# Optimization experiments

Measured on AMD Instinct MI355X. Metric: run time of the kernel, lower is better.

The kernel has to match this reference:

```python
import jax, jax.numpy as jnp
import numpy as np

D_MODEL = 1024
N_HEADS = 16
D_HEAD = D_MODEL // N_HEADS
D_FF = 4096
EPS = 1e-5


def _layernorm(x, g, b):
    mu = jnp.mean(x, axis=-1, keepdims=True)
    var = jnp.mean(jnp.square(x - mu), axis=-1, keepdims=True)
    return (x - mu) * jax.lax.rsqrt(var + EPS) * g + b


def setup_inputs() -> dict:
    key = jax.random.key(0)
    ks = jax.random.split(key, 16)
    B, S, D = 2, 2048, D_MODEL

    def xavier(k, shape):
        fan_in, fan_out = shape[0], shape[1]
        lim = float(np.sqrt(6.0 / (fan_in + fan_out)))
        return jax.random.uniform(k, shape, jnp.float32, -lim, lim)

    return {
        "x": jax.random.normal(ks[0], (B, S, D), jnp.float32),
        "ln1_g": jnp.ones((D,), jnp.float32),
        "ln1_b": jnp.zeros((D,), jnp.float32),
        "wq": xavier(ks[1], (D, D)), "bq": jnp.zeros((D,), jnp.float32),
        "wk": xavier(ks[2], (D, D)), "bk": jnp.zeros((D,), jnp.float32),
        "wv": xavier(ks[3], (D, D)), "bv": jnp.zeros((D,), jnp.float32),
        "wo": xavier(ks[4], (D, D)), "bo": jnp.zeros((D,), jnp.float32),
        "wf": xavier(ks[5], (D, N_HEADS)), "bf": jnp.zeros((N_HEADS,), jnp.float32),
        "ln2_g": jnp.ones((D,), jnp.float32),
        "ln2_b": jnp.zeros((D,), jnp.float32),
        "w1": xavier(ks[6], (D, D_FF)), "b1": jnp.zeros((D_FF,), jnp.float32),
        "w2": xavier(ks[7], (D_FF, D)), "b2": jnp.zeros((D,), jnp.float32),
    }


def reference(x, ln1_g, ln1_b, wq, bq, wk, bk, wv, bv, wo, bo, wf, bf,
              ln2_g, ln2_b, w1, b1, w2, b2):
    B, S, D = x.shape
    H, Dh = N_HEADS, D_HEAD

    # --- pre-norm forgetting attention ---
    h = _layernorm(x, ln1_g, ln1_b)
    q = (h @ wq + bq).reshape(B, S, H, Dh)
    k = (h @ wk + bk).reshape(B, S, H, Dh)
    v = (h @ wv + bv).reshape(B, S, H, Dh)

    # per-head scalar forget gate f_t in (0,1); cumulative log-decay c_t
    logf = jax.nn.log_sigmoid(h @ wf + bf)           # (B, S, H)
    c = jnp.cumsum(logf, axis=1)                     # (B, S, H)

    scale = 1.0 / jnp.sqrt(jnp.asarray(Dh, x.dtype))
    logits = jnp.einsum("bihd,bjhd->bhij", q, k) * scale
    # decay bias D_ij = c_i - c_j (sum of log forget gates in (j, i])
    decay = c.transpose(0, 2, 1)                     # (B, H, S)
    logits = logits + decay[:, :, :, None] - decay[:, :, None, :]

    causal = jnp.tril(jnp.ones((S, S), bool))
    logits = jnp.where(causal[None, None], logits, -jnp.inf)

    attn = jax.nn.softmax(logits, axis=-1)           # (B, H, S, S)
    ctx = jnp.einsum("bhij,bjhd->bihd", attn, v).reshape(B, S, D)
    attn_out = ctx @ wo + bo

    x = x + attn_out                                 # dropout = identity (eval)

    # --- pre-norm GELU MLP ---
    h2 = _layernorm(x, ln2_g, ln2_b)
    ff = jax.nn.gelu(h2 @ w1 + b1, approximate=False) @ w2 + b2
    return x + ff
```

## Files before the change

kernel.cpp:

```cpp
#include <hip/hip_runtime.h>
#include <hip/hip_bf16.h>
#include <math.h>

typedef unsigned short u16;
typedef unsigned int u32;
typedef __bf16 bf16x8 __attribute__((ext_vector_type(8)));
typedef float f32x4 __attribute__((ext_vector_type(4)));
typedef u32 u32x4 __attribute__((ext_vector_type(4)));

__device__ __forceinline__ u16 f2bf(float f) {
  __hip_bfloat16 h = __float2bfloat16(f);
  return *reinterpret_cast<u16*>(&h);
}
__device__ __forceinline__ float bf2f(u16 u) {
  return __uint_as_float(((u32)u) << 16);
}

#define GLL(gp, lp)                                                     \
  __builtin_amdgcn_global_load_lds(                                     \
      (const __attribute__((address_space(1))) void*)(gp),              \
      (__attribute__((address_space(3))) void*)(lp), 16, 0, 0)

__global__ __launch_bounds__(256) void transpose_cast(
    const float* __restrict__ in, u16* __restrict__ out, int R, int C) {
  __shared__ float tile[32][33];
  int c0 = blockIdx.x * 32, r0 = blockIdx.y * 32;
  int tx = threadIdx.x & 31, ty = threadIdx.x >> 5;
  for (int i = ty; i < 32; i += 8) {
    int r = r0 + i, c = c0 + tx;
    if (r < R && c < C) tile[i][tx] = in[(size_t)r * C + c];
  }
  __syncthreads();
  for (int i = ty; i < 32; i += 8) {
    int c = c0 + i, r = r0 + tx;
    if (c < C && r < R) out[(size_t)c * R + r] = f2bf(tile[tx][i]);
  }
}

__global__ __launch_bounds__(256) void pack3(
    const float* __restrict__ a, const float* __restrict__ b,
    const float* __restrict__ c, float* __restrict__ o, u32* __restrict__ ctr) {
  int t = blockIdx.x * 256 + threadIdx.x;
  if (t == 0) *ctr = 0u;
  if (t < 1024) o[t] = a[t];
  else if (t < 2048) o[t] = b[t - 1024];
  else if (t < 3072) o[t] = c[t - 2048];
}

__global__ __launch_bounds__(256) void ln_kernel(
    const float* __restrict__ x, const float* __restrict__ g,
    const float* __restrict__ bb, u16* __restrict__ out) {
  __shared__ float red[8];
  const int row = blockIdx.x;
  const float* xr = x + (size_t)row * 1024;
  f32x4 v = *(const f32x4*)(xr + threadIdx.x * 4);
  float s = v[0] + v[1] + v[2] + v[3];
  #pragma unroll
  for (int off = 32; off > 0; off >>= 1) s += __shfl_xor(s, off, 64);
  if ((threadIdx.x & 63) == 0) red[threadIdx.x >> 6] = s;
  __syncthreads();
  float mu = (red[0] + red[1] + red[2] + red[3]) * (1.0f / 1024.0f);
  f32x4 d;
  d[0] = v[0] - mu; d[1] = v[1] - mu; d[2] = v[2] - mu; d[3] = v[3] - mu;
  float sq = d[0]*d[0] + d[1]*d[1] + d[2]*d[2] + d[3]*d[3];
  #pragma unroll
  for (int off = 32; off > 0; off >>= 1) sq += __shfl_xor(sq, off, 64);
  if ((threadIdx.x & 63) == 0) red[4 + (threadIdx.x >> 6)] = sq;
  __syncthreads();
  float var = (red[4] + red[5] + red[6] + red[7]) * (1.0f / 1024.0f);
  float rstd = rsqrtf(var + 1e-5f);
  int cb = threadIdx.x * 4;
  #pragma unroll
  for (int e = 0; e < 4; ++e)
    out[(size_t)row * 1024 + cb + e] = f2bf(d[e] * rstd * g[cb + e] + bb[cb + e]);
}

__global__ __launch_bounds__(256) void gemm_bt(
    const u16* __restrict__ A, const u16* __restrict__ Bt,
    const float* __restrict__ bias, const float* __restrict__ res,
    void* __restrict__ outp, int M, int N, int K, int mode) {
  __shared__ u16 As[128 * 32];
  __shared__ u16 Bs[128 * 32];
  const int tid = threadIdx.x;
  const int m0 = blockIdx.y * 128, n0 = blockIdx.x * 128;
  const int wave = tid >> 6, lane = tid & 63;
  const int wm = (wave >> 1) * 64, wn = (wave & 1) * 64;
  const int lr = lane & 15, quad = lane >> 4;
  const int g0 = wave * 2;
  const int srow0 = g0 * 16 + (lane >> 2);
  const int scol = (lane & 3) * 8;
  const u16* Ag0 = A + (size_t)(m0 + srow0) * K + scol;
  const u16* Ag1 = A + (size_t)(m0 + srow0 + 16) * K + scol;
  const u16* Bg0 = Bt + (size_t)(n0 + srow0) * K + scol;
  const u16* Bg1 = Bt + (size_t)(n0 + srow0 + 16) * K + scol;
  u16* Al0 = As + g0 * 512;
  u16* Al1 = As + (g0 + 1) * 512;
  u16* Bl0 = Bs + g0 * 512;
  u16* Bl1 = Bs + (g0 + 1) * 512;

  f32x4 acc[4][4] = {};

  for (int k0 = 0; k0 < K; k0 += 32) {
    GLL(Ag0 + k0, Al0);
    GLL(Ag1 + k0, Al1);
    GLL(Bg0 + k0, Bl0);
    GLL(Bg1 + k0, Bl1);
    __syncthreads();
    bf16x8 af[4], bfr[4];
    #pragma unroll
    for (int t = 0; t < 4; ++t) {
      af[t]  = *(const bf16x8*)&As[(wm + t * 16 + lr) * 32 + quad * 8];
      bfr[t] = *(const bf16x8*)&Bs[(wn + t * 16 + lr) * 32 + quad * 8];
    }
    #pragma unroll
    for (int mt = 0; mt < 4; ++mt)
      #pragma unroll
      for (int nt = 0; nt < 4; ++nt)
        acc[mt][nt] = __builtin_amdgcn_mfma_f32_16x16x32_bf16(
            af[mt], bfr[nt], acc[mt][nt], 0, 0, 0);
    __syncthreads();
  }

  #pragma unroll
  for (int mt = 0; mt < 4; ++mt) {
    #pragma unroll
    for (int nt = 0; nt < 4; ++nt) {
      const int col = n0 + wn + nt * 16 + lr;
      const float bvv = bias[col];
      #pragma unroll
      for (int rr = 0; rr < 4; ++rr) {
        const int row = m0 + wm + mt * 16 + quad * 4 + rr;
        const size_t idx = (size_t)row * N + col;
        float v = acc[mt][nt][rr] + bvv;
        if (mode == 0) {
          ((float*)outp)[idx] = v;
        } else if (mode == 1) {
          ((float*)outp)[idx] = v + res[idx];
        } else if (mode == 2) {
          float gl = 0.5f * v * (1.0f + erff(v * 0.70710678118654752f));
          ((u16*)outp)[idx] = f2bf(gl);
        } else {
          ((u16*)outp)[idx] = f2bf(v);
        }
      }
    }
  }
}

__global__ __launch_bounds__(256) void gemm_n64(
    const u16* __restrict__ A, const u16* __restrict__ Bt,
    const float* __restrict__ bias, const float* __restrict__ res,
    void* __restrict__ outp, int M, int N, int K, int mode) {
  __shared__ u16 As[128 * 32];
  __shared__ u16 Bs[64 * 32];
  const int tid = threadIdx.x;
  const int m0 = blockIdx.y * 128, n0 = blockIdx.x * 64;
  const int wave = tid >> 6, lane = tid & 63;
  const int wm = (wave >> 1) * 64, wn = (wave & 1) * 32;
  const int lr = lane & 15, quad = lane >> 4;
  const int g0 = wave * 2;
  const int srow = lane >> 2;
  const int scol = (lane & 3) * 8;
  const u16* Ag0 = A + (size_t)(m0 + g0 * 16 + srow) * K + scol;
  const u16* Ag1 = A + (size_t)(m0 + g0 * 16 + 16 + srow) * K + scol;
  const u16* Bg  = Bt + (size_t)(n0 + wave * 16 + srow) * K + scol;
  u16* Al0 = As + g0 * 512;
  u16* Al1 = As + (g0 + 1) * 512;
  u16* Bl  = Bs + wave * 512;

  f32x4 acc[4][2] = {};

  for (int k0 = 0; k0 < K; k0 += 32) {
    GLL(Ag0 + k0, Al0);
    GLL(Ag1 + k0, Al1);
    GLL(Bg + k0, Bl);
    __syncthreads();
    bf16x8 af[4], bfr[2];
    #pragma unroll
    for (int t = 0; t < 4; ++t)
      af[t] = *(const bf16x8*)&As[(wm + t * 16 + lr) * 32 + quad * 8];
    #pragma unroll
    for (int t = 0; t < 2; ++t)
      bfr[t] = *(const bf16x8*)&Bs[(wn + t * 16 + lr) * 32 + quad * 8];
    #pragma unroll
    for (int mt = 0; mt < 4; ++mt)
      #pragma unroll
      for (int nt = 0; nt < 2; ++nt)
        acc[mt][nt] = __builtin_amdgcn_mfma_f32_16x16x32_bf16(
            af[mt], bfr[nt], acc[mt][nt], 0, 0, 0);
    __syncthreads();
  }

  #pragma unroll
  for (int mt = 0; mt < 4; ++mt) {
    #pragma unroll
    for (int nt = 0; nt < 2; ++nt) {
      const int col = n0 + wn + nt * 16 + lr;
      const float bvv = bias[col];
      #pragma unroll
      for (int rr = 0; rr < 4; ++rr) {
        const int row = m0 + wm + mt * 16 + quad * 4 + rr;
        const size_t idx = (size_t)row * N + col;
        float v = acc[mt][nt][rr] + bvv;
        if (mode == 0) {
          ((float*)outp)[idx] = v;
        } else if (mode == 1) {
          ((float*)outp)[idx] = v + res[idx];
        } else if (mode == 2) {
          float gl = 0.5f * v * (1.0f + erff(v * 0.70710678118654752f));
          ((u16*)outp)[idx] = f2bf(gl);
        } else {
          ((u16*)outp)[idx] = f2bf(v);
        }
      }
    }
  }
}

__global__ __launch_bounds__(64) void logf_kernel(
    const u16* __restrict__ h, const u16* __restrict__ wfT,
    const float* __restrict__ bfv, float* __restrict__ c) {
  const int row = blockIdx.x;
  const int lane = threadIdx.x;
  float acc[16];
  #pragma unroll
  for (int n = 0; n < 16; ++n) acc[n] = 0.f;
  for (int t = 0; t < 16; ++t) {
    int kidx = t * 64 + lane;
    float hv = bf2f(h[(size_t)row * 1024 + kidx]);
    #pragma unroll
    for (int n = 0; n < 16; ++n)
      acc[n] += hv * bf2f(wfT[n * 1024 + kidx]);
  }
  float z = 0.f;
  #pragma unroll
  for (int n = 0; n < 16; ++n) {
    float r = acc[n];
    #pragma unroll
    for (int off = 1; off < 64; off <<= 1) r += __shfl_xor(r, off, 64);
    if (lane == n) z = r;
  }
  if (lane < 16) {
    z += bfv[lane];
    float lf = (z >= 0.f) ? -log1pf(expf(-z)) : (z - log1pf(expf(z)));
    c[(size_t)row * 16 + lane] = lf;
  }
}

__global__ __launch_bounds__(64) void cumsum_kernel(float* __restrict__ c, int S) {
  const int b = blockIdx.x >> 4, h = blockIdx.x & 15;
  const int lane = threadIdx.x;
  float carry = 0.f;
  for (int s0 = 0; s0 < S; s0 += 64) {
    float v = c[(size_t)(b * S + s0 + lane) * 16 + h];
    #pragma unroll
    for (int off = 1; off < 64; off <<= 1) {
      float t = __shfl_up(v, off, 64);
      if (lane >= off) v += t;
    }
    v += carry;
    c[(size_t)(b * S + s0 + lane) * 16 + h] = v;
    carry = __shfl(v, 63, 64);
  }
}

__global__ __launch_bounds__(256) void vtrans(
    const u16* __restrict__ qkvb, u16* __restrict__ vtg) {
  __shared__ u16 t[32][33];
  const int bh = blockIdx.z, b = bh >> 4, h = bh & 15;
  const int s0 = blockIdx.x * 32, d0 = blockIdx.y * 32;
  const int tx = threadIdx.x & 31, ty = threadIdx.x >> 5;
  for (int i = ty; i < 32; i += 8)
    t[i][tx] = qkvb[(size_t)(b * 2048 + s0 + i) * 3072 + 2048 + h * 64 + d0 + tx];
  __syncthreads();
  for (int i = ty; i < 32; i += 8)
    vtg[(size_t)(bh * 64 + d0 + i) * 2048 + s0 + tx] = t[tx][i];
}

#define FS 72
#define NITEMS 1024
#define L2E 1.4426950408889634f

__global__ __launch_bounds__(256) void fattn(
    const u16* __restrict__ qkvb, const u16* __restrict__ vtg,
    const float* __restrict__ c, u16* __restrict__ ctx, u32* __restrict__ ctr) {
  __shared__ u16 Qs[64 * FS];
  __shared__ u16 Ks[64 * FS];
  __shared__ u16 Vt[64 * FS];
  __shared__ u16 Ps[64 * FS];
  __shared__ float cjs[64];
  __shared__ u32 sh_item;
  const int S = 2048;
  const int tid = threadIdx.x, wave = tid >> 6, lane = tid & 63;
  const int lr = lane & 15, quad = lane >> 4;
  const int w16 = wave * 16;
  const int sr = tid >> 2, scc = (tid & 3) * 16;

  for (;;) {
    if (tid == 0) sh_item = atomicAdd(ctr, 1u);
    __syncthreads();
    const u32 item = sh_item;
    if (item >= NITEMS) return;
    const int qt = 31 - (int)(item >> 5);
    const int bh = (int)(item & 31), b = bh >> 4, h = bh & 15;
    const int i0 = qt * 64;

    {
      const u16* src = qkvb + (size_t)(b * S + i0 + sr) * 3072 + h * 64 + scc;
      *(u32x4*)&Qs[sr * FS + scc] = *(const u32x4*)src;
      *(u32x4*)&Qs[sr * FS + scc + 8] = *(const u32x4*)(src + 8);
    }
    u32x4 kr0, kr1, vr0, vr1;
    float cjr = 0.f;
    {
      const u16* ks = qkvb + (size_t)(b * S + sr) * 3072 + 1024 + h * 64 + scc;
      kr0 = *(const u32x4*)ks;
      kr1 = *(const u32x4*)(ks + 8);
      const u16* vs = vtg + (size_t)(bh * 64 + sr) * 2048 + scc;
      vr0 = *(const u32x4*)vs;
      vr1 = *(const u32x4*)(vs + 8);
      if (tid < 64) cjr = c[(size_t)(b * S + tid) * 16 + h];
    }
    float ci[4], m_[4], l_[4], alpha[4];
    f32x4 o_[4];
    #pragma unroll
    for (int r = 0; r < 4; ++r) {
      ci[r] = c[(size_t)(b * S + i0 + w16 + quad * 4 + r) * 16 + h] * L2E;
      m_[r] = -INFINITY;
      l_[r] = 0.f;
    }
    #pragma unroll
    for (int dt = 0; dt < 4; ++dt) o_[dt] = (f32x4){0.f, 0.f, 0.f, 0.f};

    __syncthreads();
    const bf16x8 aq0 = *(const bf16x8*)&Qs[(w16 + lr) * FS + quad * 8];
    const bf16x8 aq1 = *(const bf16x8*)&Qs[(w16 + lr) * FS + 32 + quad * 8];

    const int ntiles = qt + 1;
    for (int jt = 0; jt < ntiles; ++jt) {
      const int j0 = jt * 64;
      *(u32x4*)&Ks[sr * FS + scc] = kr0;
      *(u32x4*)&Ks[sr * FS + scc + 8] = kr1;
      *(u32x4*)&Vt[sr * FS + scc] = vr0;
      *(u32x4*)&Vt[sr * FS + scc + 8] = vr1;
      if (tid < 64) cjs[tid] = cjr * L2E;
      if (jt + 1 < ntiles) {
        const int j1 = j0 + 64;
        const u16* ks = qkvb + (size_t)(b * S + j1 + sr) * 3072 + 1024 + h * 64 + scc;
        kr0 = *(const u32x4*)ks;
        kr1 = *(const u32x4*)(ks + 8);
        const u16* vs = vtg + (size_t)(bh * 64 + sr) * 2048 + j1 + scc;
        vr0 = *(const u32x4*)vs;
        vr1 = *(const u32x4*)(vs + 8);
        if (tid < 64) cjr = c[(size_t)(b * S + j1 + tid) * 16 + h];
      }
      __syncthreads();

      f32x4 sc[4];
      #pragma unroll
      for (int nt = 0; nt < 4; ++nt) {
        bf16x8 bk0 = *(const bf16x8*)&Ks[(nt * 16 + lr) * FS + quad * 8];
        bf16x8 bk1 = *(const bf16x8*)&Ks[(nt * 16 + lr) * FS + 32 + quad * 8];
        f32x4 z = {0.f, 0.f, 0.f, 0.f};
        z = __builtin_amdgcn_mfma_f32_16x16x32_bf16(aq0, bk0, z, 0, 0, 0);
        z = __builtin_amdgcn_mfma_f32_16x16x32_bf16(aq1, bk1, z, 0, 0, 0);
        sc[nt] = z;
      }
      const bool diag = (jt == qt);
      #pragma unroll
      for (int r = 0; r < 4; ++r) {
        const int i = i0 + w16 + quad * 4 + r;
        float lg[4], mrow = -INFINITY;
        #pragma unroll
        for (int nt = 0; nt < 4; ++nt) {
          const int j = j0 + nt * 16 + lr;
          float v = sc[nt][r] * (0.125f * L2E) + ci[r] - cjs[nt * 16 + lr];
          if (diag && (j > i)) v = -INFINITY;
          lg[nt] = v;
          mrow = fmaxf(mrow, v);
        }
        #pragma unroll
        for (int off = 1; off < 16; off <<= 1)
          mrow = fmaxf(mrow, __shfl_xor(mrow, off, 64));
        const float mn = fmaxf(m_[r], mrow);
        alpha[r] = __builtin_exp2f(m_[r] - mn);
        m_[r] = mn;
        float rs = 0.f;
        #pragma unroll
        for (int nt = 0; nt < 4; ++nt) {
          const float p = __builtin_exp2f(lg[nt] - mn);
          Ps[(w16 + quad * 4 + r) * FS + nt * 16 + lr] = f2bf(p);
          rs += p;
        }
        l_[r] = l_[r] * alpha[r] + rs;
      }
      asm volatile("s_waitcnt lgkmcnt(0)" ::: "memory");
      #pragma unroll
      for (int dt = 0; dt < 4; ++dt)
        #pragma unroll
        for (int r = 0; r < 4; ++r) o_[dt][r] *= alpha[r];
      bf16x8 ap0 = *(const bf16x8*)&Ps[(w16 + lr) * FS + quad * 8];
      bf16x8 ap1 = *(const bf16x8*)&Ps[(w16 + lr) * FS + 32 + quad * 8];
      #pragma unroll
      for (int dt = 0; dt < 4; ++dt) {
        bf16x8 bv0 = *(const bf16x8*)&Vt[(dt * 16 + lr) * FS + quad * 8];
        bf16x8 bv1 = *(const bf16x8*)&Vt[(dt * 16 + lr) * FS + 32 + quad * 8];
        o_[dt] = __builtin_amdgcn_mfma_f32_16x16x32_bf16(ap0, bv0, o_[dt], 0, 0, 0);
        o_[dt] = __builtin_amdgcn_mfma_f32_16x16x32_bf16(ap1, bv1, o_[dt], 0, 0, 0);
      }
      __syncthreads();
    }
    #pragma unroll
    for (int r = 0; r < 4; ++r) {
      float lt = l_[r];
      #pragma unroll
      for (int off = 1; off < 16; off <<= 1) lt += __shfl_xor(lt, off, 64);
      const float inv = 1.0f / lt;
      const size_t base = (size_t)(b * S + i0 + w16 + quad * 4 + r) * 1024 + h * 64;
      #pragma unroll
      for (int dt = 0; dt < 4; ++dt)
        ctx[base + dt * 16 + lr] = f2bf(o_[dt][r] * inv);
    }
  }
}

extern "C" void kernel_launch(void* const* d_in, const int* in_sizes, int n_in,
                              void* d_out, int out_size, void* d_ws, size_t ws_size,
                              hipStream_t stream) {
  const float* x    = (const float*)d_in[0];
  const float* ln1g = (const float*)d_in[1];
  const float* ln1b = (const float*)d_in[2];
  const float* wq   = (const float*)d_in[3];
  const float* bq   = (const float*)d_in[4];
  const float* wk   = (const float*)d_in[5];
  const float* bk   = (const float*)d_in[6];
  const float* wv   = (const float*)d_in[7];
  const float* bv   = (const float*)d_in[8];
  const float* wo   = (const float*)d_in[9];
  const float* bo   = (const float*)d_in[10];
  const float* wf   = (const float*)d_in[11];
  const float* bfv  = (const float*)d_in[12];
  const float* ln2g = (const float*)d_in[13];
  const float* ln2b = (const float*)d_in[14];
  const float* w1   = (const float*)d_in[15];
  const float* b1   = (const float*)d_in[16];
  const float* w2   = (const float*)d_in[17];
  const float* b2   = (const float*)d_in[18];
  float* out = (float*)d_out;

  char* ws = (char*)d_ws;
  const size_t MB = 1024 * 1024;
  u16*   wqkvT = (u16*)(ws + 0 * MB);
  u16*   woT   = (u16*)(ws + 6 * MB);
  u16*   w1T   = (u16*)(ws + 8 * MB);
  u16*   w2T   = (u16*)(ws + 16 * MB);
  u16*   wfT   = (u16*)(ws + 24 * MB);
  float* bqkv  = (float*)(ws + 24 * MB + 65536);
  u32*   fctr  = (u32*)(ws + 24 * MB + 131072);
  u16*   hbuf  = (u16*)(ws + 25 * MB);
  u16*   ctx   = (u16*)(ws + 33 * MB);
  u16*   qkvb  = (u16*)(ws + 41 * MB);
  u16*   vtg   = (u16*)(ws + 65 * MB);
  float* cb    = (float*)(ws + 73 * MB);
  u16*   act1  = (u16*)(ws + 74 * MB);

  dim3 blk(256);
  transpose_cast<<<dim3(32, 32), blk, 0, stream>>>(wq, wqkvT, 1024, 1024);
  transpose_cast<<<dim3(32, 32), blk, 0, stream>>>(wk, wqkvT + 1024 * 1024, 1024, 1024);
  transpose_cast<<<dim3(32, 32), blk, 0, stream>>>(wv, wqkvT + 2 * 1024 * 1024, 1024, 1024);
  transpose_cast<<<dim3(32, 32), blk, 0, stream>>>(wo, woT, 1024, 1024);
  transpose_cast<<<dim3(128, 32), blk, 0, stream>>>(w1, w1T, 1024, 4096);
  transpose_cast<<<dim3(32, 128), blk, 0, stream>>>(w2, w2T, 4096, 1024);
  transpose_cast<<<dim3(1, 32), blk, 0, stream>>>(wf, wfT, 1024, 16);
  pack3<<<12, blk, 0, stream>>>(bq, bk, bv, bqkv, fctr);
  ln_kernel<<<4096, blk, 0, stream>>>(x, ln1g, ln1b, hbuf);
  gemm_bt<<<dim3(24, 32), blk, 0, stream>>>(hbuf, wqkvT, bqkv, nullptr, qkvb,
                                            4096, 3072, 1024, 3);
  logf_kernel<<<4096, dim3(64), 0, stream>>>(hbuf, wfT, bfv, cb);
  cumsum_kernel<<<32, dim3(64), 0, stream>>>(cb, 2048);
  vtrans<<<dim3(64, 2, 32), blk, 0, stream>>>(qkvb, vtg);
  fattn<<<dim3(512), blk, 0, stream>>>(qkvb, vtg, cb, ctx, fctr);
  gemm_n64<<<dim3(16, 32), blk, 0, stream>>>(ctx, woT, bo, x, out,
                                             4096, 1024, 1024, 1);
  ln_kernel<<<4096, blk, 0, stream>>>(out, ln2g, ln2b, hbuf);
  gemm_bt<<<dim3(32, 32), blk, 0, stream>>>(hbuf, w1T, b1, nullptr, act1,
                                            4096, 4096, 1024, 2);
  gemm_n64<<<dim3(16, 32), blk, 0, stream>>>(act1, w2T, b2, out, out,
                                             4096, 1024, 4096, 1);
}
```

Measured before the change: 524.0 us.

## Skip decayed attention tiles, split-K the FFN down-projection, fuse residual into LN2

The attention kernel now walks key tiles from the diagonal backwards. It drops the query-side decay term and stops early once a bound built from the max Q/K norms and the cumulative decay says the remaining logits fall more than 40 below the running max. This removes work on tiles whose weights are negligible, at the cost of an approximation with a fixed threshold. A new qk_norms kernel computes per-tile norm maxima, and the persistent grid doubles to 1024 blocks. The second LayerNorm also writes x+b2 into the output, so the FFN down GEMM becomes a 4-way split-K with atomic float adds, trading more parallelism for atomic traffic and nondeterministic summation order.

```diff
diff --git a/kernel.cpp b/kernel.cpp
--- a/kernel.cpp
+++ b/kernel.cpp
@@ -48,8 +48,9 @@
 }
 
 __global__ __launch_bounds__(256) void ln_kernel(
-    const float* __restrict__ x, const float* __restrict__ g,
-    const float* __restrict__ bb, u16* __restrict__ out) {
+    const float* x, const float* __restrict__ g,
+    const float* __restrict__ bb, u16* __restrict__ out,
+    float* xadd, const float* addb) {
   __shared__ float red[8];
   const int row = blockIdx.x;
   const float* xr = x + (size_t)row * 1024;
@@ -73,6 +74,12 @@
   #pragma unroll
   for (int e = 0; e < 4; ++e)
     out[(size_t)row * 1024 + cb + e] = f2bf(d[e] * rstd * g[cb + e] + bb[cb + e]);
+  if (xadd) {
+    f32x4 w;
+    #pragma unroll
+    for (int e = 0; e < 4; ++e) w[e] = v[e] + addb[cb + e];
+    *(f32x4*)(xadd + (size_t)row * 1024 + cb) = w;
+  }
 }
 
 __global__ __launch_bounds__(256) void gemm_bt(
@@ -217,6 +224,65 @@
   }
 }
 
+__global__ __launch_bounds__(256) void gemm_n64_sk(
+    const u16* __restrict__ A, const u16* __restrict__ Bt,
+    float* __restrict__ outp, int M, int N, int Ktot, int Kslice) {
+  __shared__ u16 As[128 * 32];
+  __shared__ u16 Bs[64 * 32];
+  const int tid = threadIdx.x;
+  const int m0 = blockIdx.y * 128, n0 = blockIdx.x * 64;
+  const int kbeg = blockIdx.z * Kslice, kend = kbeg + Kslice;
+  const int wave = tid >> 6, lane = tid & 63;
+  const int wm = (wave >> 1) * 64, wn = (wave & 1) * 32;
+  const int lr = lane & 15, quad = lane >> 4;
+  const int g0 = wave * 2;
+  const int srow = lane >> 2;
+  const int scol = (lane & 3) * 8;
+  const u16* Ag0 = A + (size_t)(m0 + g0 * 16 + srow) * Ktot + scol;
+  const u16* Ag1 = A + (size_t)(m0 + g0 * 16 + 16 + srow) * Ktot + scol;
+  const u16* Bg  = Bt + (size_t)(n0 + wave * 16 + srow) * Ktot + scol;
+  u16* Al0 = As + g0 * 512;
+  u16* Al1 = As + (g0 + 1) * 512;
+  u16* Bl  = Bs + wave * 512;
+
+  f32x4 acc[4][2] = {};
+
+  for (int k0 = kbeg; k0 < kend; k0 += 32) {
+    GLL(Ag0 + k0, Al0);
+    GLL(Ag1 + k0, Al1);
+    GLL(Bg + k0, Bl);
+    __syncthreads();
+    bf16x8 af[4], bfr[2];
+    #pragma unroll
+    for (int t = 0; t < 4; ++t)
+      af[t] = *(const bf16x8*)&As[(wm + t * 16 + lr) * 32 + quad * 8];
+    #pragma unroll
+    for (int t = 0; t < 2; ++t)
+      bfr[t] = *(const bf16x8*)&Bs[(wn + t * 16 + lr) * 32 + quad * 8];
+    #pragma unroll
+    for (int mt = 0; mt < 4; ++mt)
+      #pragma unroll
+      for (int nt = 0; nt < 2; ++nt)
+        acc[mt][nt] = __builtin_amdgcn_mfma_f32_16x16x32_bf16(
+            af[mt], bfr[nt], acc[mt][nt], 0, 0, 0);
+    __syncthreads();
+  }
+
+  #pragma unroll
+  for (int mt = 0; mt < 4; ++mt) {
+    #pragma unroll
+    for (int nt = 0; nt < 2; ++nt) {
+      const int col = n0 + wn + nt * 16 + lr;
+      #pragma unroll
+      for (int rr = 0; rr < 4; ++rr) {
+        const int row = m0 + wm + mt * 16 + quad * 4 + rr;
+        __hip_atomic_fetch_add(&outp[(size_t)row * N + col], acc[mt][nt][rr],
+                               __ATOMIC_RELAXED, __HIP_MEMORY_SCOPE_AGENT);
+      }
+    }
+  }
+}
+
 __global__ __launch_bounds__(64) void logf_kernel(
     const u16* __restrict__ h, const u16* __restrict__ wfT,
     const float* __restrict__ bfv, float* __restrict__ c) {
@@ -277,18 +343,46 @@
     vtg[(size_t)(bh * 64 + d0 + i) * 2048 + s0 + tx] = t[tx][i];
 }
 
+__global__ __launch_bounds__(64) void qk_norms(
+    const u16* __restrict__ qkvb, float* __restrict__ qkmax) {
+  const int tile = blockIdx.x, bh = blockIdx.y, z = blockIdx.z;
+  const int b = bh >> 4, h = bh & 15;
+  const int tok = tile * 64 + (int)threadIdx.x;
+  const u16* p = qkvb + (size_t)(b * 2048 + tok) * 3072 + z * 1024 + h * 64;
+  float s = 0.f;
+  #pragma unroll
+  for (int i = 0; i < 4; ++i) {
+    u32x4 w = *(const u32x4*)(p + i * 16);
+    u32x4 w2 = *(const u32x4*)(p + i * 16 + 8);
+    #pragma unroll
+    for (int e = 0; e < 4; ++e) {
+      float lo = __uint_as_float(w[e] << 16);
+      float hi = __uint_as_float(w[e] & 0xffff0000u);
+      float lo2 = __uint_as_float(w2[e] << 16);
+      float hi2 = __uint_as_float(w2[e] & 0xffff0000u);
+      s += lo * lo + hi * hi + lo2 * lo2 + hi2 * hi2;
+    }
+  }
+  s = sqrtf(s);
+  #pragma unroll
+  for (int off = 1; off < 64; off <<= 1) s = fmaxf(s, __shfl_xor(s, off, 64));
+  if (threadIdx.x == 0) qkmax[z * 1024 + bh * 32 + tile] = s;
+}
+
 #define FS 72
 #define NITEMS 1024
 #define L2E 1.4426950408889634f
 
 __global__ __launch_bounds__(256) void fattn(
     const u16* __restrict__ qkvb, const u16* __restrict__ vtg,
-    const float* __restrict__ c, u16* __restrict__ ctx, u32* __restrict__ ctr) {
+    const float* __restrict__ c, const float* __restrict__ qkmax,
+    u16* __restrict__ ctx, u32* __restrict__ ctr) {
   __shared__ u16 Qs[64 * FS];
   __shared__ u16 Ks[64 * FS];
   __shared__ u16 Vt[64 * FS];
   __shared__ u16 Ps[64 * FS];
   __shared__ float cjs[64];
+  __shared__ float wmn[4];
   __shared__ u32 sh_item;
   const int S = 2048;
   const int tid = threadIdx.x, wave = tid >> 6, lane = tid & 63;
@@ -313,19 +407,25 @@
     u32x4 kr0, kr1, vr0, vr1;
     float cjr = 0.f;
     {
-      const u16* ks = qkvb + (size_t)(b * S + sr) * 3072 + 1024 + h * 64 + scc;
+      const u16* ks = qkvb + (size_t)(b * S + i0 + sr) * 3072 + 1024 + h * 64 + scc;
       kr0 = *(const u32x4*)ks;
       kr1 = *(const u32x4*)(ks + 8);
-      const u16* vs = vtg + (size_t)(bh * 64 + sr) * 2048 + scc;
+      const u16* vs = vtg + (size_t)(bh * 64 + sr) * 2048 + i0 + scc;
       vr0 = *(const u32x4*)vs;
       vr1 = *(const u32x4*)(vs + 8);
-      if (tid < 64) cjr = c[(size_t)(b * S + tid) * 16 + h];
-    }
-    float ci[4], m_[4], l_[4], alpha[4];
+      if (tid < 64) cjr = c[(size_t)(b * S + i0 + tid) * 16 + h];
+    }
+    float bscale;
+    {
+      float qm = qkmax[bh * 32 + qt];
+      float km = 0.f;
+      for (int t = 0; t <= qt; ++t) km = fmaxf(km, qkmax[1024 + bh * 32 + t]);
+      bscale = qm * km * (0.125f * L2E);
+    }
+    float m_[4], l_[4], alpha[4];
     f32x4 o_[4];
     #pragma unroll
     for (int r = 0; r < 4; ++r) {
-      ci[r] = c[(size_t)(b * S + i0 + w16 + quad * 4 + r) * 16 + h] * L2E;
       m_[r] = -INFINITY;
       l_[r] = 0.f;
     }
@@ -336,16 +436,15 @@
     const bf16x8 aq0 = *(const bf16x8*)&Qs[(w16 + lr) * FS + quad * 8];
     const bf16x8 aq1 = *(const bf16x8*)&Qs[(w16 + lr) * FS + 32 + quad * 8];
 
-    const int ntiles = qt + 1;
-    for (int jt = 0; jt < ntiles; ++jt) {
+    for (int jt = qt; jt >= 0; --jt) {
       const int j0 = jt * 64;
       *(u32x4*)&Ks[sr * FS + scc] = kr0;
       *(u32x4*)&Ks[sr * FS + scc + 8] = kr1;
       *(u32x4*)&Vt[sr * FS + scc] = vr0;
       *(u32x4*)&Vt[sr * FS + scc + 8] = vr1;
       if (tid < 64) cjs[tid] = cjr * L2E;
-      if (jt + 1 < ntiles) {
-        const int j1 = j0 + 64;
+      if (jt > 0) {
+        const int j1 = j0 - 64;
         const u16* ks = qkvb + (size_t)(b * S + j1 + sr) * 3072 + 1024 + h * 64 + scc;
         kr0 = *(const u32x4*)ks;
         kr1 = *(const u32x4*)(ks + 8);
@@ -374,7 +473,7 @@
         #pragma unroll
         for (int nt = 0; nt < 4; ++nt) {
           const int j = j0 + nt * 16 + lr;
-          float v = sc[nt][r] * (0.125f * L2E) + ci[r] - cjs[nt * 16 + lr];
+          float v = sc[nt][r] * (0.125f * L2E) - cjs[nt * 16 + lr];
           if (diag && (j > i)) v = -INFINITY;
           lg[nt] = v;
           mrow = fmaxf(mrow, v);
@@ -408,7 +507,18 @@
         o_[dt] = __builtin_amdgcn_mfma_f32_16x16x32_bf16(ap0, bv0, o_[dt], 0, 0, 0);
         o_[dt] = __builtin_amdgcn_mfma_f32_16x16x32_bf16(ap1, bv1, o_[dt], 0, 0, 0);
       }
+      {
+        float wmin = fminf(fminf(m_[0], m_[1]), fminf(m_[2], m_[3]));
+        wmin = fminf(wmin, __shfl_xor(wmin, 16, 64));
+        wmin = fminf(wmin, __shfl_xor(wmin, 32, 64));
+        if (lane == 0) wmn[wave] = wmin;
+      }
       __syncthreads();
+      if (jt > 0) {
+        const float bmin = fminf(fminf(wmn[0], wmn[1]), fminf(wmn[2], wmn[3]));
+        const float cend = c[(size_t)(b * S + j0 - 1) * 16 + h];
+        if (bscale - cend * L2E < bmin - 40.f) break;
+      }
     }
     #pragma unroll
     for (int r = 0; r < 4; ++r) {
@@ -462,6 +572,7 @@
   u16*   qkvb  = (u16*)(ws + 41 * MB);
   u16*   vtg   = (u16*)(ws + 65 * MB);
   float* cb    = (float*)(ws + 73 * MB);
+  float* qkmax = (float*)(ws + 73 * MB + 262144);
   u16*   act1  = (u16*)(ws + 74 * MB);
 
   dim3 blk(256);
@@ -473,18 +584,19 @@
   transpose_cast<<<dim3(32, 128), blk, 0, stream>>>(w2, w2T, 4096, 1024);
   transpose_cast<<<dim3(1, 32), blk, 0, stream>>>(wf, wfT, 1024, 16);
   pack3<<<12, blk, 0, stream>>>(bq, bk, bv, bqkv, fctr);
-  ln_kernel<<<4096, blk, 0, stream>>>(x, ln1g, ln1b, hbuf);
+  ln_kernel<<<4096, blk, 0, stream>>>(x, ln1g, ln1b, hbuf, nullptr, nullptr);
   gemm_bt<<<dim3(24, 32), blk, 0, stream>>>(hbuf, wqkvT, bqkv, nullptr, qkvb,
                                             4096, 3072, 1024, 3);
   logf_kernel<<<4096, dim3(64), 0, stream>>>(hbuf, wfT, bfv, cb);
   cumsum_kernel<<<32, dim3(64), 0, stream>>>(cb, 2048);
   vtrans<<<dim3(64, 2, 32), blk, 0, stream>>>(qkvb, vtg);
-  fattn<<<dim3(512), blk, 0, stream>>>(qkvb, vtg, cb, ctx, fctr);
+  qk_norms<<<dim3(32, 32, 2), dim3(64), 0, stream>>>(qkvb, qkmax);
+  fattn<<<dim3(1024), blk, 0, stream>>>(qkvb, vtg, cb, qkmax, ctx, fctr);
   gemm_n64<<<dim3(16, 32), blk, 0, stream>>>(ctx, woT, bo, x, out,
                                              4096, 1024, 1024, 1);
-  ln_kernel<<<4096, blk, 0, stream>>>(out, ln2g, ln2b, hbuf);
+  ln_kernel<<<4096, blk, 0, stream>>>(out, ln2g, ln2b, hbuf, out, b2);
   gemm_bt<<<dim3(32, 32), blk, 0, stream>>>(hbuf, w1T, b1, nullptr, act1,
                                             4096, 4096, 1024, 2);
-  gemm_n64<<<dim3(16, 32), blk, 0, stream>>>(act1, w2T, b2, out, out,
-                                             4096, 1024, 4096, 1);
-}
+  gemm_n64_sk<<<dim3(16, 32, 4), blk, 0, stream>>>(act1, w2T, out,
+                                                   4096, 1024, 4096, 1024);
+}
```

Result: faster. 498.7 us (-4.8%).
